# Performance work log

Hardware: AMD Instinct MI355X
Metric: run time of the kernel (lower is better)

Reference implementation:

```python
import jax, jax.numpy as jnp
import numpy as np

N_AGENTS, HIDDEN, MSG, KEY = 8192, 256, 128, 64

def _glorot(k, shape):
    fan_in, fan_out = shape[0], shape[1]
    lim = jnp.sqrt(6.0 / (fan_in + fan_out))
    return jax.random.uniform(k, shape, jnp.float32, -lim, lim)

def setup_inputs() -> dict:
    key = jax.random.key(0)
    ks = jax.random.split(key, 12)
    inp = {
        'h': jax.random.normal(ks[0], (N_AGENTS, HIDDEN), jnp.float32),
        'W_msg': _glorot(ks[1], (HIDDEN, MSG)), 'b_msg': jnp.zeros((MSG,), jnp.float32),
        'W_key': _glorot(ks[2], (HIDDEN, KEY)), 'b_key': jnp.zeros((KEY,), jnp.float32),
        'W_qry': _glorot(ks[3], (HIDDEN, KEY)), 'b_qry': jnp.zeros((KEY,), jnp.float32),
        # GRUCell: input (attended message, dim MSG) -> hidden; gates r,z,n
        'Wi_r': _glorot(ks[4], (MSG, HIDDEN)), 'bi_r': jnp.zeros((HIDDEN,), jnp.float32),
        'Wi_z': _glorot(ks[5], (MSG, HIDDEN)), 'bi_z': jnp.zeros((HIDDEN,), jnp.float32),
        'Wi_n': _glorot(ks[6], (MSG, HIDDEN)), 'bi_n': jnp.zeros((HIDDEN,), jnp.float32),
        'Wh_r': _glorot(ks[7], (HIDDEN, HIDDEN)),
        'Wh_z': _glorot(ks[8], (HIDDEN, HIDDEN)),
        'Wh_n': _glorot(ks[9], (HIDDEN, HIDDEN)), 'bh_n': jnp.zeros((HIDDEN,), jnp.float32),
    }
    return inp

def reference(h, W_msg, b_msg, W_key, b_key, W_qry, b_qry,
              Wi_r, bi_r, Wi_z, bi_z, Wi_n, bi_n, Wh_r, Wh_z, Wh_n, bh_n):
    n = h.shape[0]
    messages = h @ W_msg + b_msg            # [N, MSG]
    keys = h @ W_key + b_key                # [N, KEY]
    queries = h @ W_qry + b_qry             # [N, KEY]
    scale = jnp.sqrt(jnp.float32(keys.shape[-1]))
    scores = (queries @ keys.T) / scale     # [N, N]
    scores = jnp.clip(scores, -20.0, 20.0)
    self_mask = jnp.eye(n, dtype=scores.dtype)
    scores = jnp.where(self_mask > 0, -1e8, scores)
    attn_weights = jax.nn.softmax(scores, axis=-1)
    attended = attn_weights @ messages      # [N, MSG]
    # flax GRUCell: carry = h, inputs = attended
    r = jax.nn.sigmoid(attended @ Wi_r + bi_r + h @ Wh_r)
    z = jax.nn.sigmoid(attended @ Wi_z + bi_z + h @ Wh_z)
    cand = jnp.tanh(attended @ Wi_n + bi_n + r * (h @ Wh_n + bh_n))
    h_new = (1.0 - z) * cand + z * h
    return (h_new, attn_weights)
```

## Files before the change

kernel.cpp:

```cpp
#include <hip/hip_runtime.h>
#include <math.h>

#define N_AGENTS 8192
#define HIDDEN   256
#define MSG      128
#define KEYD     64
#define CSPLIT   8

#define OFF_WM_H   0
#define OFF_WM_L   32768
#define OFF_WK_H   65536
#define OFF_WK_L   81920
#define OFF_WQ_H   98304
#define OFF_WQ_L   114688
#define OFF_WIR_H  131072
#define OFF_WIR_L  163840
#define OFF_WIZ_H  196608
#define OFF_WIZ_L  229376
#define OFF_WIN_H  262144
#define OFF_WIN_L  294912
#define OFF_WHR_H  327680
#define OFF_WHR_L  393216
#define OFF_WHZ_H  458752
#define OFF_WHZ_L  524288
#define OFF_WHN_H  589824
#define OFF_WHN_L  655360
#define WT_TOTAL   720896

typedef __attribute__((ext_vector_type(8))) short short8_t;
typedef __attribute__((ext_vector_type(4))) short short4_t;
typedef __attribute__((ext_vector_type(4))) float float4_t;

__device__ __forceinline__ short f2bf(float x) {
    unsigned u = __float_as_uint(x);
    unsigned r = (u + 0x7fffu + ((u >> 16) & 1u)) >> 16;
    return (short)r;
}
__device__ __forceinline__ float bf2f(short b) {
    return __uint_as_float(((unsigned)(unsigned short)b) << 16);
}
__device__ __forceinline__ void split4(float4 v, short4_t* hi, short4_t* lo) {
    (*hi)[0] = f2bf(v.x); (*lo)[0] = f2bf(v.x - bf2f((*hi)[0]));
    (*hi)[1] = f2bf(v.y); (*lo)[1] = f2bf(v.y - bf2f((*hi)[1]));
    (*hi)[2] = f2bf(v.z); (*lo)[2] = f2bf(v.z - bf2f((*hi)[2]));
    (*hi)[3] = f2bf(v.w); (*lo)[3] = f2bf(v.w - bf2f((*hi)[3]));
}

__global__ __launch_bounds__(256) void prep_weights(
    const float* __restrict__ Wm, const float* __restrict__ Wk, const float* __restrict__ Wq,
    const float* __restrict__ Wir, const float* __restrict__ Wiz, const float* __restrict__ Win,
    const float* __restrict__ Whr, const float* __restrict__ Whz, const float* __restrict__ Whn,
    short* __restrict__ wT)
{
    int idx = blockIdx.x * 256 + threadIdx.x;
    const float* src; int K, lgC, local; size_t oh, ol;
    if (idx < 32768)        { src = Wm;  K = 256; lgC = 7; local = idx;          oh = OFF_WM_H;  ol = OFF_WM_L; }
    else if (idx < 49152)   { src = Wk;  K = 256; lgC = 6; local = idx - 32768;  oh = OFF_WK_H;  ol = OFF_WK_L; }
    else if (idx < 65536)   { src = Wq;  K = 256; lgC = 6; local = idx - 49152;  oh = OFF_WQ_H;  ol = OFF_WQ_L; }
    else if (idx < 98304)   { src = Wir; K = 128; lgC = 8; local = idx - 65536;  oh = OFF_WIR_H; ol = OFF_WIR_L; }
    else if (idx < 131072)  { src = Wiz; K = 128; lgC = 8; local = idx - 98304;  oh = OFF_WIZ_H; ol = OFF_WIZ_L; }
    else if (idx < 163840)  { src = Win; K = 128; lgC = 8; local = idx - 131072; oh = OFF_WIN_H; ol = OFF_WIN_L; }
    else if (idx < 229376)  { src = Whr; K = 256; lgC = 8; local = idx - 163840; oh = OFF_WHR_H; ol = OFF_WHR_L; }
    else if (idx < 294912)  { src = Whz; K = 256; lgC = 8; local = idx - 229376; oh = OFF_WHZ_H; ol = OFF_WHZ_L; }
    else if (idx < 360448)  { src = Whn; K = 256; lgC = 8; local = idx - 294912; oh = OFF_WHN_H; ol = OFF_WHN_L; }
    else return;
    int k = local >> lgC, c = local & ((1 << lgC) - 1);
    float v = src[local];
    short hi = f2bf(v);
    short lo = f2bf(v - bf2f(hi));
    wT[oh + (size_t)c * K + k] = hi;
    wT[ol + (size_t)c * K + k] = lo;
}

__global__ __launch_bounds__(256) void proj_mfma_kernel(
    const float* __restrict__ h, const short* __restrict__ wT,
    const float* __restrict__ bm, const float* __restrict__ bk, const float* __restrict__ bq,
    short* __restrict__ msgTb,
    short* __restrict__ qh, short* __restrict__ ql,
    short* __restrict__ kh, short* __restrict__ kl)
{
    __shared__ short hh[16][264], hl[16][264];
    int t = threadIdx.x;
    int wave = t >> 6, l = t & 63, quad = l >> 4, ln = l & 15;
    int i0 = blockIdx.x * 16;

#pragma unroll
    for (int p = 0; p < 4; p++) {
        int idx = t + p * 256;
        int r = idx >> 6, k4 = (idx & 63) * 4;
        float4 v = *(const float4*)&h[(size_t)(i0 + r) * HIDDEN + k4];
        short4_t hv, lv;
        split4(v, &hv, &lv);
        *(short4_t*)&hh[r][k4] = hv;
        *(short4_t*)&hl[r][k4] = lv;
    }
    __syncthreads();

    size_t base_h, base_l; int cb;
    if (wave < 2)      { base_h = OFF_WM_H; base_l = OFF_WM_L; cb = wave * 64; }
    else if (wave == 2){ base_h = OFF_WK_H; base_l = OFF_WK_L; cb = 0; }
    else               { base_h = OFF_WQ_H; base_l = OFF_WQ_L; cb = 0; }

    float4_t acc[4];
#pragma unroll
    for (int nt = 0; nt < 4; nt++) acc[nt] = (float4_t)0.f;

    for (int ch = 0; ch < 8; ch++) {
        short8_t a_h = *(short8_t*)&hh[ln][ch * 32 + quad * 8];
        short8_t a_l = *(short8_t*)&hl[ln][ch * 32 + quad * 8];
#pragma unroll
        for (int nt = 0; nt < 4; nt++) {
            int c = cb + nt * 16 + ln;
            const short* bp_h = wT + base_h + (size_t)c * 256 + ch * 32 + quad * 8;
            const short* bp_l = wT + base_l + (size_t)c * 256 + ch * 32 + quad * 8;
            short8_t b_h = *(const short8_t*)bp_h;
            short8_t b_l = *(const short8_t*)bp_l;
            acc[nt] = __builtin_amdgcn_mfma_f32_16x16x32_bf16(a_h, b_h, acc[nt], 0, 0, 0);
            acc[nt] = __builtin_amdgcn_mfma_f32_16x16x32_bf16(a_h, b_l, acc[nt], 0, 0, 0);
            acc[nt] = __builtin_amdgcn_mfma_f32_16x16x32_bf16(a_l, b_h, acc[nt], 0, 0, 0);
        }
    }

    if (wave < 2) {
#pragma unroll
        for (int nt = 0; nt < 4; nt++) {
            int col = cb + nt * 16 + ln;
            float b = bm[col];
            short4_t o;
#pragma unroll
            for (int reg = 0; reg < 4; reg++) o[reg] = f2bf(acc[nt][reg] + b);
            *(short4_t*)&msgTb[(size_t)col * N_AGENTS + i0 + quad * 4] = o;
        }
    } else {
        short* dh = (wave == 2) ? kh : qh;
        short* dl = (wave == 2) ? kl : ql;
        const float* bias = (wave == 2) ? bk : bq;
#pragma unroll
        for (int nt = 0; nt < 4; nt++) {
            int col = nt * 16 + ln;
            float b = bias[col];
#pragma unroll
            for (int reg = 0; reg < 4; reg++) {
                int row = i0 + quad * 4 + reg;
                float v = acc[nt][reg] + b;
                short hi = f2bf(v);
                short lo = f2bf(v - bf2f(hi));
                dh[(size_t)row * KEYD + col] = hi;
                dl[(size_t)row * KEYD + col] = lo;
            }
        }
    }
}

__global__ __launch_bounds__(256) void rowsum_kernel(
    const short* __restrict__ qh, const short* __restrict__ ql,
    const short* __restrict__ kh, const short* __restrict__ kl,
    float* __restrict__ rowsum)
{
    int t = threadIdx.x;
    int wave = t >> 6, l = t & 63;
    int quad = l >> 4, ln = l & 15;
    int i0 = blockIdx.y * 64;
    int j0 = blockIdx.x * 256 + wave * 64;

    short8_t ah[4][2], al[4][2];
#pragma unroll
    for (int r = 0; r < 4; r++)
#pragma unroll
        for (int ch = 0; ch < 2; ch++) {
            size_t off = (size_t)(i0 + r * 16 + ln) * KEYD + ch * 32 + quad * 8;
            ah[r][ch] = *(const short8_t*)(qh + off);
            al[r][ch] = *(const short8_t*)(ql + off);
        }

    float4_t acc[4][4];
#pragma unroll
    for (int r = 0; r < 4; r++)
#pragma unroll
        for (int c = 0; c < 4; c++) acc[r][c] = (float4_t)0.f;

#pragma unroll
    for (int c = 0; c < 4; c++) {
        int coln = j0 + c * 16 + ln;
#pragma unroll
        for (int ch = 0; ch < 2; ch++) {
            size_t off = (size_t)coln * KEYD + ch * 32 + quad * 8;
            short8_t bh = *(const short8_t*)(kh + off);
            short8_t bl = *(const short8_t*)(kl + off);
#pragma unroll
            for (int r = 0; r < 4; r++) {
                acc[r][c] = __builtin_amdgcn_mfma_f32_16x16x32_bf16(ah[r][ch], bh, acc[r][c], 0, 0, 0);
                acc[r][c] = __builtin_amdgcn_mfma_f32_16x16x32_bf16(ah[r][ch], bl, acc[r][c], 0, 0, 0);
                acc[r][c] = __builtin_amdgcn_mfma_f32_16x16x32_bf16(al[r][ch], bh, acc[r][c], 0, 0, 0);
            }
        }
    }

    float prow[4][4];
#pragma unroll
    for (int r = 0; r < 4; r++)
#pragma unroll
        for (int reg = 0; reg < 4; reg++) {
            int gi = i0 + r * 16 + quad * 4 + reg;
            float sum = 0.f;
#pragma unroll
            for (int c = 0; c < 4; c++) {
                float s = acc[r][c][reg] * 0.125f;
                s = fminf(fmaxf(s, -20.f), 20.f);
                int gj = j0 + c * 16 + ln;
                float p = (gi == gj) ? 0.f : __expf(s);
                sum += p;
            }
            prow[r][reg] = sum;
        }

#pragma unroll
    for (int off = 1; off < 16; off <<= 1)
#pragma unroll
        for (int r = 0; r < 4; r++)
#pragma unroll
            for (int reg = 0; reg < 4; reg++)
                prow[r][reg] += __shfl_xor(prow[r][reg], off);

    if (ln == 0) {
#pragma unroll
        for (int r = 0; r < 4; r++)
#pragma unroll
            for (int reg = 0; reg < 4; reg++)
                atomicAdd(&rowsum[i0 + r * 16 + quad * 4 + reg], prow[r][reg]);
    }
}

__global__ __launch_bounds__(256) void attend_fused_kernel(
    const short* __restrict__ qh, const short* __restrict__ ql,
    const short* __restrict__ kh, const short* __restrict__ kl,
    const short* __restrict__ msgTb, const float* __restrict__ rowsum,
    float* __restrict__ P, float* __restrict__ att)
{
    const int JB = 128;
    const int STR = JB + 8;
    __shared__ short A_lds[64][STR];
    __shared__ short B_lds[MSG][STR];
    __shared__ float inv_s[64];

    int t = threadIdx.x;
    int wave = t >> 6, l = t & 63;
    int quad = l >> 4, ln = l & 15;
    int i0 = blockIdx.y * 64;
    int kbase = blockIdx.x * (N_AGENTS / CSPLIT);

    if (t < 64) inv_s[t] = 1.0f / rowsum[i0 + t];

    short8_t ah[4][2], al[4][2];
#pragma unroll
    for (int r = 0; r < 4; r++)
#pragma unroll
        for (int ch = 0; ch < 2; ch++) {
            size_t off = (size_t)(i0 + r * 16 + ln) * KEYD + ch * 32 + quad * 8;
            ah[r][ch] = *(const short8_t*)(qh + off);
            al[r][ch] = *(const short8_t*)(ql + off);
        }

    float4_t accm[8];
#pragma unroll
    for (int c = 0; c < 8; c++) accm[c] = (float4_t)0.f;

    __syncthreads();

    for (int jt = 0; jt < N_AGENTS / CSPLIT; jt += JB) {
        int kpos = kbase + jt;

        float4_t acc[4][2];
#pragma unroll
        for (int r = 0; r < 4; r++)
#pragma unroll
            for (int c2 = 0; c2 < 2; c2++) acc[r][c2] = (float4_t)0.f;

#pragma unroll
        for (int c2 = 0; c2 < 2; c2++) {
            int coln = kpos + wave * 32 + c2 * 16 + ln;
#pragma unroll
            for (int ch = 0; ch < 2; ch++) {
                size_t off = (size_t)coln * KEYD + ch * 32 + quad * 8;
                short8_t bh = *(const short8_t*)(kh + off);
                short8_t bl = *(const short8_t*)(kl + off);
#pragma unroll
                for (int r = 0; r < 4; r++) {
                    acc[r][c2] = __builtin_amdgcn_mfma_f32_16x16x32_bf16(ah[r][ch], bh, acc[r][c2], 0, 0, 0);
                    acc[r][c2] = __builtin_amdgcn_mfma_f32_16x16x32_bf16(ah[r][ch], bl, acc[r][c2], 0, 0, 0);
                    acc[r][c2] = __builtin_amdgcn_mfma_f32_16x16x32_bf16(al[r][ch], bh, acc[r][c2], 0, 0, 0);
                }
            }
        }

        __syncthreads();

        short8_t bst[8];
#pragma unroll
        for (int p = 0; p < 8; p++) {
            int idx = t + p * 256;
            int c = idx >> 4, kk = (idx & 15) * 8;
            bst[p] = *(const short8_t*)(msgTb + (size_t)c * N_AGENTS + kpos + kk);
        }

#pragma unroll
        for (int r = 0; r < 4; r++)
#pragma unroll
            for (int reg = 0; reg < 4; reg++) {
                int row = r * 16 + quad * 4 + reg;
                int gi = i0 + row;
                float iv = inv_s[row];
#pragma unroll
                for (int c2 = 0; c2 < 2; c2++) {
                    int col = wave * 32 + c2 * 16 + ln;
                    int gj = kpos + col;
                    float s = acc[r][c2][reg] * 0.125f;
                    s = fminf(fmaxf(s, -20.f), 20.f);
                    float p = (gi == gj) ? 0.f : __expf(s) * iv;
                    __builtin_nontemporal_store(p, &P[(size_t)gi * N_AGENTS + gj]);
                    A_lds[row][col] = f2bf(p);
                }
            }

#pragma unroll
        for (int p = 0; p < 8; p++) {
            int idx = t + p * 256;
            int c = idx >> 4, kk = (idx & 15) * 8;
            *(short8_t*)&B_lds[c][kk] = bst[p];
        }

        __syncthreads();

#pragma unroll
        for (int kc = 0; kc < 4; kc++) {
            short8_t a = *(short8_t*)&A_lds[wave * 16 + ln][kc * 32 + quad * 8];
#pragma unroll
            for (int c = 0; c < 8; c++) {
                short8_t b = *(short8_t*)&B_lds[c * 16 + ln][kc * 32 + quad * 8];
                accm[c] = __builtin_amdgcn_mfma_f32_16x16x32_bf16(a, b, accm[c], 0, 0, 0);
            }
        }
    }

#pragma unroll
    for (int c = 0; c < 8; c++)
#pragma unroll
        for (int reg = 0; reg < 4; reg++) {
            int row = i0 + wave * 16 + quad * 4 + reg;
            int col = c * 16 + ln;
            atomicAdd(&att[(size_t)row * MSG + col], accm[c][reg]);
        }
}

__global__ __launch_bounds__(256) void gru_mfma_kernel(
    const float* __restrict__ att, const float* __restrict__ h,
    const short* __restrict__ wT,
    const float* __restrict__ bir, const float* __restrict__ biz,
    const float* __restrict__ bin, const float* __restrict__ bhn,
    float* __restrict__ hnew)
{
    __shared__ short ath[16][136], atl[16][136];
    __shared__ short hh[16][264], hl[16][264];
    int t = threadIdx.x;
    int wave = t >> 6, l = t & 63, quad = l >> 4, ln = l & 15;
    int i0 = blockIdx.x * 16;
    int cb = wave * 64;

#pragma unroll
    for (int p = 0; p < 2; p++) {
        int idx = t + p * 256;
        int r = idx >> 5, c4 = (idx & 31) * 4;
        float4 v = *(const float4*)&att[(size_t)(i0 + r) * MSG + c4];
        short4_t hv, lv;
        split4(v, &hv, &lv);
        *(short4_t*)&ath[r][c4] = hv;
        *(short4_t*)&atl[r][c4] = lv;
    }
#pragma unroll
    for (int p = 0; p < 4; p++) {
        int idx = t + p * 256;
        int r = idx >> 6, k4 = (idx & 63) * 4;
        float4 v = *(const float4*)&h[(size_t)(i0 + r) * HIDDEN + k4];
        short4_t hv, lv;
        split4(v, &hv, &lv);
        *(short4_t*)&hh[r][k4] = hv;
        *(short4_t*)&hl[r][k4] = lv;
    }
    __syncthreads();

    float4_t ar[4], az[4], an[4], hn[4];
#pragma unroll
    for (int nt = 0; nt < 4; nt++) {
        ar[nt] = (float4_t)0.f; az[nt] = (float4_t)0.f;
        an[nt] = (float4_t)0.f; hn[nt] = (float4_t)0.f;
    }

#define MFMA3(ACC, AH, AL, BH, BL)                                              \
    ACC = __builtin_amdgcn_mfma_f32_16x16x32_bf16(AH, BH, ACC, 0, 0, 0);        \
    ACC = __builtin_amdgcn_mfma_f32_16x16x32_bf16(AH, BL, ACC, 0, 0, 0);        \
    ACC = __builtin_amdgcn_mfma_f32_16x16x32_bf16(AL, BH, ACC, 0, 0, 0);

    for (int ch = 0; ch < 4; ch++) {
        short8_t a_h = *(short8_t*)&ath[ln][ch * 32 + quad * 8];
        short8_t a_l = *(short8_t*)&atl[ln][ch * 32 + quad * 8];
#pragma unroll
        for (int nt = 0; nt < 4; nt++) {
            size_t cw = (size_t)(cb + nt * 16 + ln) * 128 + ch * 32 + quad * 8;
            short8_t brh = *(const short8_t*)(wT + OFF_WIR_H + cw);
            short8_t brl = *(const short8_t*)(wT + OFF_WIR_L + cw);
            MFMA3(ar[nt], a_h, a_l, brh, brl);
            short8_t bzh = *(const short8_t*)(wT + OFF_WIZ_H + cw);
            short8_t bzl = *(const short8_t*)(wT + OFF_WIZ_L + cw);
            MFMA3(az[nt], a_h, a_l, bzh, bzl);
            short8_t bnh = *(const short8_t*)(wT + OFF_WIN_H + cw);
            short8_t bnl = *(const short8_t*)(wT + OFF_WIN_L + cw);
            MFMA3(an[nt], a_h, a_l, bnh, bnl);
        }
    }

    for (int ch = 0; ch < 8; ch++) {
        short8_t a_h = *(short8_t*)&hh[ln][ch * 32 + quad * 8];
        short8_t a_l = *(short8_t*)&hl[ln][ch * 32 + quad * 8];
#pragma unroll
        for (int nt = 0; nt < 4; nt++) {
            size_t cw = (size_t)(cb + nt * 16 + ln) * 256 + ch * 32 + quad * 8;
            short8_t brh = *(const short8_t*)(wT + OFF_WHR_H + cw);
            short8_t brl = *(const short8_t*)(wT + OFF_WHR_L + cw);
            MFMA3(ar[nt], a_h, a_l, brh, brl);
            short8_t bzh = *(const short8_t*)(wT + OFF_WHZ_H + cw);
            short8_t bzl = *(const short8_t*)(wT + OFF_WHZ_L + cw);
            MFMA3(az[nt], a_h, a_l, bzh, bzl);
            short8_t bnh = *(const short8_t*)(wT + OFF_WHN_H + cw);
            short8_t bnl = *(const short8_t*)(wT + OFF_WHN_L + cw);
            MFMA3(hn[nt], a_h, a_l, bnh, bnl);
        }
    }
#undef MFMA3

#pragma unroll
    for (int nt = 0; nt < 4; nt++) {
        int col = cb + nt * 16 + ln;
        float br = bir[col], bz = biz[col], bn = bin[col], bh_ = bhn[col];
#pragma unroll
        for (int reg = 0; reg < 4; reg++) {
            int row = i0 + quad * 4 + reg;
            float hv = h[(size_t)row * HIDDEN + col];
            float rr = 1.f / (1.f + __expf(-(ar[nt][reg] + br)));
            float zz = 1.f / (1.f + __expf(-(az[nt][reg] + bz)));
            float cand = tanhf(an[nt][reg] + bn + rr * (hn[nt][reg] + bh_));
            hnew[(size_t)row * HIDDEN + col] = (1.f - zz) * cand + zz * hv;
        }
    }
}

extern "C" void kernel_launch(void* const* d_in, const int* in_sizes, int n_in,
                              void* d_out, int out_size, void* d_ws, size_t ws_size,
                              hipStream_t stream)
{
    const float* h     = (const float*)d_in[0];
    const float* W_msg = (const float*)d_in[1];
    const float* b_msg = (const float*)d_in[2];
    const float* W_key = (const float*)d_in[3];
    const float* b_key = (const float*)d_in[4];
    const float* W_qry = (const float*)d_in[5];
    const float* b_qry = (const float*)d_in[6];
    const float* Wi_r  = (const float*)d_in[7];
    const float* bi_r  = (const float*)d_in[8];
    const float* Wi_z  = (const float*)d_in[9];
    const float* bi_z  = (const float*)d_in[10];
    const float* Wi_n  = (const float*)d_in[11];
    const float* bi_n  = (const float*)d_in[12];
    const float* Wh_r  = (const float*)d_in[13];
    const float* Wh_z  = (const float*)d_in[14];
    const float* Wh_n  = (const float*)d_in[15];
    const float* bh_n  = (const float*)d_in[16];

    float* out  = (float*)d_out;
    float* hnew = out;
    float* P    = out + (size_t)N_AGENTS * HIDDEN;

    float* ws     = (float*)d_ws;
    float* rowsum = ws;
    float* att    = ws + N_AGENTS;
    short* sbase  = (short*)(att + (size_t)N_AGENTS * MSG);
    short* msgTb  = sbase;
    short* qh     = msgTb + (size_t)MSG * N_AGENTS;
    short* ql     = qh + (size_t)N_AGENTS * KEYD;
    short* kh     = ql + (size_t)N_AGENTS * KEYD;
    short* kl     = kh + (size_t)N_AGENTS * KEYD;
    short* wT     = kl + (size_t)N_AGENTS * KEYD;

    hipMemsetAsync(d_ws, 0, (size_t)(N_AGENTS + (size_t)N_AGENTS * MSG) * sizeof(float), stream);

    prep_weights<<<1408, 256, 0, stream>>>(W_msg, W_key, W_qry, Wi_r, Wi_z, Wi_n,
                                           Wh_r, Wh_z, Wh_n, wT);

    proj_mfma_kernel<<<N_AGENTS / 16, 256, 0, stream>>>(h, wT, b_msg, b_key, b_qry,
                                                        msgTb, qh, ql, kh, kl);

    rowsum_kernel<<<dim3(N_AGENTS / 256, N_AGENTS / 64), 256, 0, stream>>>(qh, ql, kh, kl, rowsum);

    attend_fused_kernel<<<dim3(CSPLIT, N_AGENTS / 64), 256, 0, stream>>>(qh, ql, kh, kl,
                                                                         msgTb, rowsum, P, att);

    gru_mfma_kernel<<<N_AGENTS / 16, 256, 0, stream>>>(att, h, wT, bi_r, bi_z, bi_n, bh_n, hnew);
}
```

Baseline: 609.9 us.

## Replace attended atomics with per-split partial buffers reduced in GRU kernel

The attend kernel now writes its per-column-split partial results to separate workspace slices instead of atomically adding into one buffer. The GRU kernel sums those partials on load, which also removes the large memset of the attended buffer. The column split drops from 8 to 4, so each block covers more columns and there are fewer partials. The P stores are moved after the LDS barrier so they can overlap with the second MFMA stage. In exchange, fewer blocks are launched and each block does a longer serial loop.

Measured after the change: 595.8 us. 1.02x faster.

```diff
diff --git a/kernel.cpp b/kernel.cpp
--- a/kernel.cpp
+++ b/kernel.cpp
@@ -5,7 +5,7 @@
 #define HIDDEN   256
 #define MSG      128
 #define KEYD     64
-#define CSPLIT   8
+#define CSPLIT   4
 
 #define OFF_WM_H   0
 #define OFF_WM_L   32768
@@ -235,7 +235,7 @@
     const short* __restrict__ qh, const short* __restrict__ ql,
     const short* __restrict__ kh, const short* __restrict__ kl,
     const short* __restrict__ msgTb, const float* __restrict__ rowsum,
-    float* __restrict__ P, float* __restrict__ att)
+    float* __restrict__ P, float* __restrict__ att_part)
 {
     const int JB = 128;
     const int STR = JB + 8;
@@ -303,6 +303,7 @@
             bst[p] = *(const short8_t*)(msgTb + (size_t)c * N_AGENTS + kpos + kk);
         }
 
+        float pv[4][4][2];
 #pragma unroll
         for (int r = 0; r < 4; r++)
 #pragma unroll
@@ -317,7 +318,7 @@
                     float s = acc[r][c2][reg] * 0.125f;
                     s = fminf(fmaxf(s, -20.f), 20.f);
                     float p = (gi == gj) ? 0.f : __expf(s) * iv;
-                    __builtin_nontemporal_store(p, &P[(size_t)gi * N_AGENTS + gj]);
+                    pv[r][reg][c2] = p;
                     A_lds[row][col] = f2bf(p);
                 }
             }
@@ -332,6 +333,18 @@
         __syncthreads();
 
 #pragma unroll
+        for (int r = 0; r < 4; r++)
+#pragma unroll
+            for (int reg = 0; reg < 4; reg++) {
+                int gi = i0 + r * 16 + quad * 4 + reg;
+#pragma unroll
+                for (int c2 = 0; c2 < 2; c2++) {
+                    int gj = kpos + wave * 32 + c2 * 16 + ln;
+                    __builtin_nontemporal_store(pv[r][reg][c2], &P[(size_t)gi * N_AGENTS + gj]);
+                }
+            }
+
+#pragma unroll
         for (int kc = 0; kc < 4; kc++) {
             short8_t a = *(short8_t*)&A_lds[wave * 16 + ln][kc * 32 + quad * 8];
 #pragma unroll
@@ -342,18 +355,19 @@
         }
     }
 
+    float* ap = att_part + (size_t)blockIdx.x * N_AGENTS * MSG;
 #pragma unroll
     for (int c = 0; c < 8; c++)
 #pragma unroll
         for (int reg = 0; reg < 4; reg++) {
             int row = i0 + wave * 16 + quad * 4 + reg;
             int col = c * 16 + ln;
-            atomicAdd(&att[(size_t)row * MSG + col], accm[c][reg]);
+            ap[(size_t)row * MSG + col] = accm[c][reg];
         }
 }
 
 __global__ __launch_bounds__(256) void gru_mfma_kernel(
-    const float* __restrict__ att, const float* __restrict__ h,
+    const float* __restrict__ att_part, const float* __restrict__ h,
     const short* __restrict__ wT,
     const float* __restrict__ bir, const float* __restrict__ biz,
     const float* __restrict__ bin, const float* __restrict__ bhn,
@@ -370,7 +384,13 @@
     for (int p = 0; p < 2; p++) {
         int idx = t + p * 256;
         int r = idx >> 5, c4 = (idx & 31) * 4;
-        float4 v = *(const float4*)&att[(size_t)(i0 + r) * MSG + c4];
+        size_t off = (size_t)(i0 + r) * MSG + c4;
+        float4 v = *(const float4*)&att_part[off];
+#pragma unroll
+        for (int s = 1; s < CSPLIT; s++) {
+            float4 w = *(const float4*)&att_part[(size_t)s * N_AGENTS * MSG + off];
+            v.x += w.x; v.y += w.y; v.z += w.z; v.w += w.w;
+        }
         short4_t hv, lv;
         split4(v, &hv, &lv);
         *(short4_t*)&ath[r][c4] = hv;
@@ -479,18 +499,18 @@
     float* hnew = out;
     float* P    = out + (size_t)N_AGENTS * HIDDEN;
 
-    float* ws     = (float*)d_ws;
-    float* rowsum = ws;
-    float* att    = ws + N_AGENTS;
-    short* sbase  = (short*)(att + (size_t)N_AGENTS * MSG);
-    short* msgTb  = sbase;
-    short* qh     = msgTb + (size_t)MSG * N_AGENTS;
-    short* ql     = qh + (size_t)N_AGENTS * KEYD;
-    short* kh     = ql + (size_t)N_AGENTS * KEYD;
-    short* kl     = kh + (size_t)N_AGENTS * KEYD;
-    short* wT     = kl + (size_t)N_AGENTS * KEYD;
-
-    hipMemsetAsync(d_ws, 0, (size_t)(N_AGENTS + (size_t)N_AGENTS * MSG) * sizeof(float), stream);
+    float* ws       = (float*)d_ws;
+    float* rowsum   = ws;
+    float* att_part = ws + N_AGENTS;
+    short* sbase    = (short*)(att_part + (size_t)CSPLIT * N_AGENTS * MSG);
+    short* msgTb    = sbase;
+    short* qh       = msgTb + (size_t)MSG * N_AGENTS;
+    short* ql       = qh + (size_t)N_AGENTS * KEYD;
+    short* kh       = ql + (size_t)N_AGENTS * KEYD;
+    short* kl       = kh + (size_t)N_AGENTS * KEYD;
+    short* wT       = kl + (size_t)N_AGENTS * KEYD;
+
+    hipMemsetAsync(rowsum, 0, (size_t)N_AGENTS * sizeof(float), stream);
 
     prep_weights<<<1408, 256, 0, stream>>>(W_msg, W_key, W_qry, Wi_r, Wi_z, Wi_n,
                                            Wh_r, Wh_z, Wh_n, wT);
@@ -501,7 +521,7 @@
     rowsum_kernel<<<dim3(N_AGENTS / 256, N_AGENTS / 64), 256, 0, stream>>>(qh, ql, kh, kl, rowsum);
 
     attend_fused_kernel<<<dim3(CSPLIT, N_AGENTS / 64), 256, 0, stream>>>(qh, ql, kh, kl,
-                                                                         msgTb, rowsum, P, att);
-
-    gru_mfma_kernel<<<N_AGENTS / 16, 256, 0, stream>>>(att, h, wT, bi_r, bi_z, bi_n, bh_n, hnew);
-}
+                                                                         msgTb, rowsum, P, att_part);
+
+    gru_mfma_kernel<<<N_AGENTS / 16, 256, 0, stream>>>(att_part, h, wT, bi_r, bi_z, bi_n, bh_n, hnew);
+}
```
